# Optimization experiments

Hardware: AMD Instinct MI355X
Metric: run time of the kernel (lower is better)

The kernel has to match this reference:

```python
import jax, jax.numpy as jnp
import numpy as np

EPS = 1e-08  # matches torch default eps in both F.normalize and PairwiseDistance


def setup_inputs() -> dict:
    key = jax.random.key(0)
    x = jax.random.normal(key, (8192, 1024), dtype=jnp.float32)
    return {"x": x}


def reference(x) -> jnp.ndarray:
    B = x.shape[0]
    # F.normalize(x, p=2, dim=-1, eps=EPS): x / max(||x||_2, eps)
    norms = jnp.linalg.norm(x, axis=-1, keepdims=True)
    xn = x / jnp.maximum(norms, EPS)
    # cosine similarity matrix [B, B]
    cos_sim = xn @ xn.T
    # fill_diagonal_(-2): exclude self from nearest-neighbor search
    idx = jnp.arange(B)
    cos_sim = cos_sim.at[idx, idx].set(-2.0)
    nn_idx = jnp.argmax(cos_sim, axis=1)  # [B] int
    # torch PairwiseDistance(p=2, eps=EPS): ||x1 - x2 + eps||_2
    diff = xn - xn[nn_idx] + EPS
    nn_dist = jnp.sqrt(jnp.sum(diff * diff, axis=-1))  # [B]
    loss = -jnp.mean(jnp.log(nn_dist + EPS))
    return loss
```

## Files before the change

### kernel.cpp

```cpp
#include <hip/hip_runtime.h>
#include <hip/hip_bf16.h>
#include <math.h>

#define NB 8192
#define ND 1024
#define KEPS 1e-8f
#define SLOTS 128
#define NTILE 32
#define NWG 528
#define NKT 16

typedef __attribute__((ext_vector_type(8))) __bf16 bf16x8;
typedef __attribute__((ext_vector_type(4))) float f32x4;

__device__ __forceinline__ unsigned int fmono(float f) {
    unsigned int b = __float_as_uint(f);
    return b ^ ((b & 0x80000000u) ? 0xFFFFFFFFu : 0x80000000u);
}
__device__ __forceinline__ unsigned short f2bf(float f) {
    union { float f; unsigned int u; } a;
    a.f = f;
    unsigned int lsb = (a.u >> 16) & 1u;
    a.u += 0x7fffu + lsb;
    return (unsigned short)(a.u >> 16);
}
__device__ __forceinline__ void gload_lds16(const void* g, void* l) {
    __builtin_amdgcn_global_load_lds(
        (const __attribute__((address_space(1))) unsigned int*)g,
        (__attribute__((address_space(3))) unsigned int*)l, 16, 0, 0);
}
__device__ __forceinline__ unsigned long long packmax(float mx, int mc) {
    return ((unsigned long long)fmono(mx) << 32) |
           (unsigned long long)(~(unsigned int)mc);
}

__global__ __launch_bounds__(256) void normalize_k(const float* __restrict__ x,
                                                   unsigned short* __restrict__ xnb) {
    int row = blockIdx.x;
    int t = threadIdx.x;
    float4 v = ((const float4*)(x + (size_t)row * ND))[t];
    float ss = v.x * v.x + v.y * v.y + v.z * v.z + v.w * v.w;
#pragma unroll
    for (int off = 32; off > 0; off >>= 1) ss += __shfl_down(ss, off, 64);
    __shared__ float sred[4];
    if ((t & 63) == 0) sred[t >> 6] = ss;
    __syncthreads();
    float tot = sred[0] + sred[1] + sred[2] + sred[3];
    float scale = 1.0f / fmaxf(sqrtf(tot), KEPS);
    ushort4 o;
    o.x = f2bf(v.x * scale);
    o.y = f2bf(v.y * scale);
    o.z = f2bf(v.z * scale);
    o.w = f2bf(v.w * scale);
    ((ushort4*)xnb)[(size_t)row * (ND / 4) + t] = o;
}

#define FENCE_BARRIER() do { asm volatile("" ::: "memory"); \
    __builtin_amdgcn_s_barrier(); asm volatile("" ::: "memory"); } while (0)
#define WAIT_VM2() asm volatile("s_waitcnt vmcnt(2)" ::: "memory")
#define WAIT_VM0() asm volatile("s_waitcnt vmcnt(0)" ::: "memory")

#define STAGE_HALF(H, DBB) do { \
    gload_lds16(sp[H][0], ldsb + (DBB) + ((H) >> 1) * 32768 + ((H) & 1) * 16384 + (0 * 8 + wv) * 1024); \
    gload_lds16(sp[H][1], ldsb + (DBB) + ((H) >> 1) * 32768 + ((H) & 1) * 16384 + (1 * 8 + wv) * 1024); \
    sp[H][0] += 128; sp[H][1] += 128; } while (0)

#define LOAD_A(MH) do { \
    const char* Ab_ = ldsb + cbB + wM * 16384 + laneA; \
    _Pragma("unroll") for (int mi = 0; mi < 4; ++mi) \
    _Pragma("unroll") for (int ks = 0; ks < 2; ++ks) \
        af[mi][ks] = *(const bf16x8*)(Ab_ + ((((MH) * 4 + mi) * 2 + ks) * 1024)); } while (0)

#define LOAD_B(BANK, NH) do { \
    const char* Bb_ = ldsb + cbB + 32768 + (wN >> 1) * 16384 + laneA; \
    _Pragma("unroll") for (int ni = 0; ni < 2; ++ni) \
    _Pragma("unroll") for (int ks = 0; ks < 2; ++ks) \
        BANK[ni][ks] = *(const bf16x8*)(Bb_ + ((((wN & 1) * 4 + (NH) * 2 + ni) * 2 + ks) * 1024)); } while (0)

#define MFMAQ(MH, NH, BANK) do { \
    __builtin_amdgcn_s_setprio(1); \
    _Pragma("unroll") for (int mi = 0; mi < 4; ++mi) \
    _Pragma("unroll") for (int ni = 0; ni < 2; ++ni) { \
        acc[(MH) * 4 + mi][(NH) * 2 + ni] = __builtin_amdgcn_mfma_f32_16x16x32_bf16( \
            af[mi][0], BANK[ni][0], acc[(MH) * 4 + mi][(NH) * 2 + ni], 0, 0, 0); \
        acc[(MH) * 4 + mi][(NH) * 2 + ni] = __builtin_amdgcn_mfma_f32_16x16x32_bf16( \
            af[mi][1], BANK[ni][1], acc[(MH) * 4 + mi][(NH) * 2 + ni], 0, 0, 0); } \
    __builtin_amdgcn_s_setprio(0); } while (0)

__global__ __launch_bounds__(512, 2) void argmax_gemm(const unsigned short* __restrict__ xnb,
                                                      unsigned long long* __restrict__ partial) {
    extern __shared__ char ldsb[];

    int wg = (int)blockIdx.x;
    int tile = (wg & 7) * (NWG / 8) + (wg >> 3);
    int by = 0, tr = tile;
    while (tr >= NTILE - by) { tr -= NTILE - by; ++by; }
    const int bx = by + tr;

    const int rowBase = by * 256, colBase = bx * 256;
    const int tid = (int)threadIdx.x;
    const int wv = tid >> 6;
    const int l = tid & 63;
    const int wM = wv >> 2;
    const int wN = wv & 3;

    const int laneA = (l & 15) * 64 + (((l >> 4) * 16) ^ ((l & 8) << 2));

    const int scb = ((l & 3) * 16) ^ ((l >> 5) << 5);
    const int srow = (l >> 2) & 15;

    const char* xb = (const char*)xnb;
    const char* sp[4][2];
#pragma unroll
    for (int h = 0; h < 4; ++h)
#pragma unroll
        for (int q = 0; q < 2; ++q) {
            int s = q * 8 + wv;
            int rgrp = s >> 1, kgrp = s & 1;
            int panel = (h >> 1) ? colBase : rowBase;
            long long grow = panel + (h & 1) * 128 + rgrp * 16 + srow;
            sp[h][q] = xb + grow * (ND * 2) + kgrp * 64 + scb;
        }

    f32x4 acc[8][4];
#pragma unroll
    for (int m = 0; m < 8; ++m)
#pragma unroll
        for (int n = 0; n < 4; ++n) acc[m][n] = f32x4{0.f, 0.f, 0.f, 0.f};

    STAGE_HALF(0, 0); STAGE_HALF(1, 0); STAGE_HALF(2, 0); STAGE_HALF(3, 0);

    int cbB = 0, dbB = 65536;
    for (int c = 0; c < NKT; ++c) {
        const bool pf = (c + 1 < NKT);
        bf16x8 af[4][2], b0[2][2], b1[2][2];
        if (pf) { STAGE_HALF(0, dbB); WAIT_VM2(); } else { WAIT_VM0(); }
        FENCE_BARRIER();
        LOAD_A(0); LOAD_B(b0, 0);
        MFMAQ(0, 0, b0);
        if (pf) STAGE_HALF(1, dbB);
        LOAD_B(b1, 1);
        MFMAQ(0, 1, b1);
        if (pf) STAGE_HALF(2, dbB);
        LOAD_A(1);
        MFMAQ(1, 1, b1);
        if (pf) STAGE_HALF(3, dbB);
        MFMAQ(1, 0, b0);
        FENCE_BARRIER();
        int tmp = cbB; cbB = dbB; dbB = tmp;
    }

#pragma unroll
    for (int m = 0; m < 8; ++m) {
#pragma unroll
        for (int r = 0; r < 4; ++r) {
            int gi = rowBase + wM * 128 + m * 16 + (l >> 4) * 4 + r;
            float mx = -3.0f;
            int mc = 0x7FFFFFFF;
#pragma unroll
            for (int n = 0; n < 4; ++n) {
                int gj = colBase + wN * 64 + n * 16 + (l & 15);
                float v = (gi == gj) ? -2.0f : acc[m][n][r];
                if (v > mx) { mx = v; mc = gj; }
            }
#pragma unroll
            for (int off = 1; off < 16; off <<= 1) {
                float omx = __shfl_xor(mx, off, 64);
                int omc = __shfl_xor(mc, off, 64);
                if (omx > mx || (omx == mx && omc < mc)) { mx = omx; mc = omc; }
            }
            if ((l & 15) == 0)
                partial[(size_t)gi * SLOTS + (2 * by + (bx - by) * 4 + wN)] = packmax(mx, mc);
        }
    }
    if (bx > by) {
#pragma unroll
        for (int n = 0; n < 4; ++n) {
            int gj = colBase + wN * 64 + n * 16 + (l & 15);
            float mx = -3.0f;
            int mc = 0x7FFFFFFF;
#pragma unroll
            for (int m = 0; m < 8; ++m) {
#pragma unroll
                for (int r = 0; r < 4; ++r) {
                    int gi = rowBase + wM * 128 + m * 16 + (l >> 4) * 4 + r;
                    float v = (gi == gj) ? -2.0f : acc[m][n][r];
                    if (v > mx) { mx = v; mc = gi; }
                }
            }
#pragma unroll
            for (int off = 16; off < 64; off <<= 1) {
                float omx = __shfl_xor(mx, off, 64);
                int omc = __shfl_xor(mc, off, 64);
                if (omx > mx || (omx == mx && omc < mc)) { mx = omx; mc = omc; }
            }
            if ((l >> 4) == 0)
                partial[(size_t)gj * SLOTS + (2 * by + wM)] = packmax(mx, mc);
        }
    }
}

__global__ __launch_bounds__(256) void dist_k(const float* __restrict__ x,
                                              const unsigned long long* __restrict__ partial,
                                              float* __restrict__ rowloss) {
    int i = blockIdx.x;
    int t = threadIdx.x;
    int nv = SLOTS - 2 * (i >> 8);
    unsigned long long p = 0ull;
    if (t < nv) p = partial[(size_t)i * SLOTS + t];
#pragma unroll
    for (int off = 1; off < 64; off <<= 1) {
        unsigned long long o = __shfl_xor(p, off, 64);
        if (o > p) p = o;
    }
    __shared__ unsigned long long sp_[4];
    __shared__ int sj;
    if ((t & 63) == 0) sp_[t >> 6] = p;
    __syncthreads();
    if (t == 0) {
        unsigned long long b = sp_[0];
        for (int k = 1; k < 4; ++k)
            if (sp_[k] > b) b = sp_[k];
        sj = (int)(~(unsigned int)(b & 0xFFFFFFFFull));
    }
    __syncthreads();
    int j = sj;

    float4 a = ((const float4*)(x + (size_t)i * ND))[t];
    float4 b = ((const float4*)(x + (size_t)j * ND))[t];
    float sa = a.x * a.x + a.y * a.y + a.z * a.z + a.w * a.w;
    float sb = b.x * b.x + b.y * b.y + b.z * b.z + b.w * b.w;
#pragma unroll
    for (int off = 32; off > 0; off >>= 1) {
        sa += __shfl_down(sa, off, 64);
        sb += __shfl_down(sb, off, 64);
    }
    __shared__ float sra[4], srb[4];
    if ((t & 63) == 0) { sra[t >> 6] = sa; srb[t >> 6] = sb; }
    __syncthreads();
    float na = sra[0] + sra[1] + sra[2] + sra[3];
    float nb = srb[0] + srb[1] + srb[2] + srb[3];
    float ia = 1.0f / fmaxf(sqrtf(na), KEPS);
    float ib = 1.0f / fmaxf(sqrtf(nb), KEPS);
    float dx = a.x * ia - b.x * ib + KEPS;
    float dy = a.y * ia - b.y * ib + KEPS;
    float dz = a.z * ia - b.z * ib + KEPS;
    float dw = a.w * ia - b.w * ib + KEPS;
    float ss = dx * dx + dy * dy + dz * dz + dw * dw;
#pragma unroll
    for (int off = 32; off > 0; off >>= 1) ss += __shfl_down(ss, off, 64);
    __shared__ float srd[4];
    if ((t & 63) == 0) srd[t >> 6] = ss;
    __syncthreads();
    if (t == 0) {
        float tot = srd[0] + srd[1] + srd[2] + srd[3];
        rowloss[i] = -logf(sqrtf(tot) + KEPS);
    }
}

__global__ __launch_bounds__(1024) void reduce_k(const float* __restrict__ rowloss,
                                                 float* __restrict__ out) {
    int t = threadIdx.x;
    float s = 0.0f;
#pragma unroll
    for (int k = 0; k < 8; ++k) s += rowloss[t + k * 1024];
#pragma unroll
    for (int off = 32; off > 0; off >>= 1) s += __shfl_down(s, off, 64);
    __shared__ float sred[16];
    if ((t & 63) == 0) sred[t >> 6] = s;
    __syncthreads();
    if (t == 0) {
        float tot = 0.0f;
        for (int k = 0; k < 16; ++k) tot += sred[k];
        out[0] = tot / (float)NB;
    }
}

extern "C" void kernel_launch(void* const* d_in, const int* in_sizes, int n_in,
                              void* d_out, int out_size, void* d_ws, size_t ws_size,
                              hipStream_t stream) {
    const float* x = (const float*)d_in[0];
    float* out = (float*)d_out;

    char* ws = (char*)d_ws;
    unsigned short* xnb = (unsigned short*)ws;
    unsigned long long* partial =
        (unsigned long long*)(ws + (size_t)NB * ND * 2);
    float* rowloss = (float*)(ws + (size_t)NB * ND * 2 + (size_t)NB * SLOTS * 8);

    (void)hipFuncSetAttribute((const void*)argmax_gemm,
                              hipFuncAttributeMaxDynamicSharedMemorySize, 131072);

    normalize_k<<<NB, 256, 0, stream>>>(x, xnb);
    argmax_gemm<<<NWG, 512, 131072, stream>>>(xnb, partial);
    dist_k<<<NB, 256, 0, stream>>>(x, partial, rowloss);
    reduce_k<<<1, 1024, 0, stream>>>(rowloss, out);
}
```

Before: 209.6 us.

## Rework GEMM LDS layout and staging schedule; make normalize/dist one row per wave

The argmax GEMM gets a new LDS layout with an XOR swizzle and new per-lane row and k offsets. Its main loop is unrolled into explicit k-tile macros that interleave global-to-LDS staging with MFMA quarters, using extra barriers, explicit lgkmcnt waits and a deeper vmcnt wait to pipeline prefetch. The normalize and distance kernels now process one row per wavefront with four float4 loads per lane and shuffle-only reductions, removing shared-memory syncs and cutting block count. The many extra barriers and the hand-tuned wait counts risk stalls or hazards if the counts are wrong.

```diff
diff --git a/kernel.cpp b/kernel.cpp
--- a/kernel.cpp
+++ b/kernel.cpp
@@ -36,46 +36,54 @@
 
 __global__ __launch_bounds__(256) void normalize_k(const float* __restrict__ x,
                                                    unsigned short* __restrict__ xnb) {
-    int row = blockIdx.x;
-    int t = threadIdx.x;
-    float4 v = ((const float4*)(x + (size_t)row * ND))[t];
-    float ss = v.x * v.x + v.y * v.y + v.z * v.z + v.w * v.w;
-#pragma unroll
-    for (int off = 32; off > 0; off >>= 1) ss += __shfl_down(ss, off, 64);
-    __shared__ float sred[4];
-    if ((t & 63) == 0) sred[t >> 6] = ss;
-    __syncthreads();
-    float tot = sred[0] + sred[1] + sred[2] + sred[3];
-    float scale = 1.0f / fmaxf(sqrtf(tot), KEPS);
-    ushort4 o;
-    o.x = f2bf(v.x * scale);
-    o.y = f2bf(v.y * scale);
-    o.z = f2bf(v.z * scale);
-    o.w = f2bf(v.w * scale);
-    ((ushort4*)xnb)[(size_t)row * (ND / 4) + t] = o;
+    int row = blockIdx.x * 4 + (threadIdx.x >> 6);
+    int l = threadIdx.x & 63;
+    const float4* xr = (const float4*)(x + (size_t)row * ND);
+    float4 v[4];
+    float ss = 0.f;
+#pragma unroll
+    for (int q = 0; q < 4; ++q) {
+        v[q] = xr[q * 64 + l];
+        ss += v[q].x * v[q].x + v[q].y * v[q].y + v[q].z * v[q].z + v[q].w * v[q].w;
+    }
+#pragma unroll
+    for (int off = 1; off < 64; off <<= 1) ss += __shfl_xor(ss, off, 64);
+    float scale = 1.0f / fmaxf(sqrtf(ss), KEPS);
+    ushort4* o = (ushort4*)(xnb + (size_t)row * ND);
+#pragma unroll
+    for (int q = 0; q < 4; ++q) {
+        ushort4 u;
+        u.x = f2bf(v[q].x * scale);
+        u.y = f2bf(v[q].y * scale);
+        u.z = f2bf(v[q].z * scale);
+        u.w = f2bf(v[q].w * scale);
+        o[q * 64 + l] = u;
+    }
 }
 
 #define FENCE_BARRIER() do { asm volatile("" ::: "memory"); \
     __builtin_amdgcn_s_barrier(); asm volatile("" ::: "memory"); } while (0)
-#define WAIT_VM2() asm volatile("s_waitcnt vmcnt(2)" ::: "memory")
+#define LGKM0() do { asm volatile("s_waitcnt lgkmcnt(0)" ::: "memory"); \
+    __builtin_amdgcn_sched_barrier(0); } while (0)
+#define WAIT_VM6() asm volatile("s_waitcnt vmcnt(6)" ::: "memory")
 #define WAIT_VM0() asm volatile("s_waitcnt vmcnt(0)" ::: "memory")
 
-#define STAGE_HALF(H, DBB) do { \
-    gload_lds16(sp[H][0], ldsb + (DBB) + ((H) >> 1) * 32768 + ((H) & 1) * 16384 + (0 * 8 + wv) * 1024); \
-    gload_lds16(sp[H][1], ldsb + (DBB) + ((H) >> 1) * 32768 + ((H) & 1) * 16384 + (1 * 8 + wv) * 1024); \
+#define STAGE(H, DB) do { \
+    gload_lds16(sp[H][0], ldsb + (DB) + (H) * 16384 + wv * 1024); \
+    gload_lds16(sp[H][1], ldsb + (DB) + (H) * 16384 + 8192 + wv * 1024); \
     sp[H][0] += 128; sp[H][1] += 128; } while (0)
 
-#define LOAD_A(MH) do { \
-    const char* Ab_ = ldsb + cbB + wM * 16384 + laneA; \
-    _Pragma("unroll") for (int mi = 0; mi < 4; ++mi) \
-    _Pragma("unroll") for (int ks = 0; ks < 2; ++ks) \
-        af[mi][ks] = *(const bf16x8*)(Ab_ + ((((MH) * 4 + mi) * 2 + ks) * 1024)); } while (0)
-
-#define LOAD_B(BANK, NH) do { \
-    const char* Bb_ = ldsb + cbB + 32768 + (wN >> 1) * 16384 + laneA; \
-    _Pragma("unroll") for (int ni = 0; ni < 2; ++ni) \
-    _Pragma("unroll") for (int ks = 0; ks < 2; ++ks) \
-        BANK[ni][ks] = *(const bf16x8*)(Bb_ + ((((wN & 1) * 4 + (NH) * 2 + ni) * 2 + ks) * 1024)); } while (0)
+#define LOAD_A(CB, MQ) do { \
+    const char* Ab_ = ldsb + (CB) + ((MQ) * 2 + wM) * 8192 + rowOff; \
+    _Pragma("unroll") for (int mi = 0; mi < 4; ++mi) { \
+        af[mi][0] = *(const bf16x8*)(Ab_ + mi * 2048 + ks0); \
+        af[mi][1] = *(const bf16x8*)(Ab_ + mi * 2048 + ks1); } } while (0)
+
+#define LOAD_B(CB, BANK, NQ) do { \
+    const char* Bb_ = ldsb + (CB) + 32768 + (NQ) * 16384 + wN * 4096 + rowOff; \
+    _Pragma("unroll") for (int ni = 0; ni < 2; ++ni) { \
+        BANK[ni][0] = *(const bf16x8*)(Bb_ + ni * 2048 + ks0); \
+        BANK[ni][1] = *(const bf16x8*)(Bb_ + ni * 2048 + ks1); } } while (0)
 
 #define MFMAQ(MH, NH, BANK) do { \
     __builtin_amdgcn_s_setprio(1); \
@@ -87,6 +95,32 @@
             af[mi][1], BANK[ni][1], acc[(MH) * 4 + mi][(NH) * 2 + ni], 0, 0, 0); } \
     __builtin_amdgcn_s_setprio(0); } while (0)
 
+#define KTILE(CB, DB, S1, S2, FINAL) do { \
+    bf16x8 af[4][2], b0[2][2], b1[2][2]; \
+    LOAD_A(CB, 0); LOAD_B(CB, b0, 0); \
+    if (S1) STAGE(1, DB); \
+    FENCE_BARRIER(); LGKM0(); MFMAQ(0, 0, b0); FENCE_BARRIER(); \
+    LOAD_B(CB, b1, 1); \
+    if (S2) STAGE(0, CB); \
+    FENCE_BARRIER(); LGKM0(); MFMAQ(0, 1, b1); FENCE_BARRIER(); \
+    LOAD_A(CB, 1); \
+    if (S2) STAGE(2, CB); \
+    FENCE_BARRIER(); LGKM0(); MFMAQ(1, 1, b1); FENCE_BARRIER(); \
+    if (S2) STAGE(3, CB); \
+    FENCE_BARRIER(); MFMAQ(1, 0, b0); \
+    if (FINAL) { WAIT_VM0(); } else { WAIT_VM6(); } \
+    FENCE_BARRIER(); } while (0)
+
+#define KTILE_LAST(CB) do { \
+    bf16x8 af[4][2], b0[2][2], b1[2][2]; \
+    LOAD_A(CB, 0); LOAD_B(CB, b0, 0); \
+    FENCE_BARRIER(); LGKM0(); MFMAQ(0, 0, b0); FENCE_BARRIER(); \
+    LOAD_B(CB, b1, 1); \
+    FENCE_BARRIER(); LGKM0(); MFMAQ(0, 1, b1); FENCE_BARRIER(); \
+    LOAD_A(CB, 1); \
+    FENCE_BARRIER(); LGKM0(); MFMAQ(1, 1, b1); FENCE_BARRIER(); \
+    MFMAQ(1, 0, b0); } while (0)
+
 __global__ __launch_bounds__(512, 2) void argmax_gemm(const unsigned short* __restrict__ xnb,
                                                       unsigned long long* __restrict__ partial) {
     extern __shared__ char ldsb[];
@@ -104,23 +138,23 @@
     const int wM = wv >> 2;
     const int wN = wv & 3;
 
-    const int laneA = (l & 15) * 64 + (((l >> 4) * 16) ^ ((l & 8) << 2));
-
-    const int scb = ((l & 3) * 16) ^ ((l >> 5) << 5);
-    const int srow = (l >> 2) & 15;
-
+    const int rowOff = (l & 15) * 128;
+    const int ks0 = (((l >> 4) * 16)) ^ ((l & 7) << 4);
+    const int ks1 = (64 | ((l >> 4) * 16)) ^ ((l & 7) << 4);
+
+    const int scol = (((l & 7) ^ (l >> 3)) << 4);
     const char* xb = (const char*)xnb;
     const char* sp[4][2];
 #pragma unroll
-    for (int h = 0; h < 4; ++h)
-#pragma unroll
-        for (int q = 0; q < 2; ++q) {
-            int s = q * 8 + wv;
-            int rgrp = s >> 1, kgrp = s & 1;
-            int panel = (h >> 1) ? colBase : rowBase;
-            long long grow = panel + (h & 1) * 128 + rgrp * 16 + srow;
-            sp[h][q] = xb + grow * (ND * 2) + kgrp * 64 + scb;
-        }
+    for (int q = 0; q < 2; ++q) {
+        int R = (q * 8 + wv) * 8 + (l >> 3);
+        int arow = (R >> 6) * 128 + (R & 63);
+        int bcol = (R >> 5) * 64 + (R & 31);
+        sp[0][q] = xb + (size_t)(rowBase + arow) * 2048 + scol;
+        sp[1][q] = xb + (size_t)(rowBase + arow + 64) * 2048 + scol;
+        sp[2][q] = xb + (size_t)(colBase + bcol) * 2048 + scol;
+        sp[3][q] = xb + (size_t)(colBase + bcol + 32) * 2048 + scol;
+    }
 
     f32x4 acc[8][4];
 #pragma unroll
@@ -128,27 +162,19 @@
 #pragma unroll
         for (int n = 0; n < 4; ++n) acc[m][n] = f32x4{0.f, 0.f, 0.f, 0.f};
 
-    STAGE_HALF(0, 0); STAGE_HALF(1, 0); STAGE_HALF(2, 0); STAGE_HALF(3, 0);
-
-    int cbB = 0, dbB = 65536;
-    for (int c = 0; c < NKT; ++c) {
-        const bool pf = (c + 1 < NKT);
-        bf16x8 af[4][2], b0[2][2], b1[2][2];
-        if (pf) { STAGE_HALF(0, dbB); WAIT_VM2(); } else { WAIT_VM0(); }
-        FENCE_BARRIER();
-        LOAD_A(0); LOAD_B(b0, 0);
-        MFMAQ(0, 0, b0);
-        if (pf) STAGE_HALF(1, dbB);
-        LOAD_B(b1, 1);
-        MFMAQ(0, 1, b1);
-        if (pf) STAGE_HALF(2, dbB);
-        LOAD_A(1);
-        MFMAQ(1, 1, b1);
-        if (pf) STAGE_HALF(3, dbB);
-        MFMAQ(1, 0, b0);
-        FENCE_BARRIER();
-        int tmp = cbB; cbB = dbB; dbB = tmp;
-    }
+    STAGE(0, 0); STAGE(2, 0); STAGE(3, 0); STAGE(1, 0);
+    STAGE(0, 65536); STAGE(2, 65536); STAGE(3, 65536);
+    WAIT_VM6();
+    FENCE_BARRIER();
+
+    for (int c = 0; c < 12; c += 2) {
+        KTILE(0, 65536, true, true, false);
+        KTILE(65536, 0, true, true, false);
+    }
+    KTILE(0, 65536, true, true, false);
+    KTILE(65536, 0, true, true, false);
+    KTILE(0, 65536, true, false, true);
+    KTILE_LAST(65536);
 
 #pragma unroll
     for (int m = 0; m < 8; ++m) {
@@ -203,59 +229,52 @@
 __global__ __launch_bounds__(256) void dist_k(const float* __restrict__ x,
                                               const unsigned long long* __restrict__ partial,
                                               float* __restrict__ rowloss) {
-    int i = blockIdx.x;
-    int t = threadIdx.x;
+    int i = blockIdx.x * 4 + (threadIdx.x >> 6);
+    int l = threadIdx.x & 63;
     int nv = SLOTS - 2 * (i >> 8);
     unsigned long long p = 0ull;
-    if (t < nv) p = partial[(size_t)i * SLOTS + t];
+    if (l < nv) p = partial[(size_t)i * SLOTS + l];
+    if (l + 64 < nv) {
+        unsigned long long o = partial[(size_t)i * SLOTS + l + 64];
+        if (o > p) p = o;
+    }
 #pragma unroll
     for (int off = 1; off < 64; off <<= 1) {
         unsigned long long o = __shfl_xor(p, off, 64);
         if (o > p) p = o;
     }
-    __shared__ unsigned long long sp_[4];
-    __shared__ int sj;
-    if ((t & 63) == 0) sp_[t >> 6] = p;
-    __syncthreads();
-    if (t == 0) {
-        unsigned long long b = sp_[0];
-        for (int k = 1; k < 4; ++k)
-            if (sp_[k] > b) b = sp_[k];
-        sj = (int)(~(unsigned int)(b & 0xFFFFFFFFull));
-    }
-    __syncthreads();
-    int j = sj;
-
-    float4 a = ((const float4*)(x + (size_t)i * ND))[t];
-    float4 b = ((const float4*)(x + (size_t)j * ND))[t];
-    float sa = a.x * a.x + a.y * a.y + a.z * a.z + a.w * a.w;
-    float sb = b.x * b.x + b.y * b.y + b.z * b.z + b.w * b.w;
-#pragma unroll
-    for (int off = 32; off > 0; off >>= 1) {
-        sa += __shfl_down(sa, off, 64);
-        sb += __shfl_down(sb, off, 64);
-    }
-    __shared__ float sra[4], srb[4];
-    if ((t & 63) == 0) { sra[t >> 6] = sa; srb[t >> 6] = sb; }
-    __syncthreads();
-    float na = sra[0] + sra[1] + sra[2] + sra[3];
-    float nb = srb[0] + srb[1] + srb[2] + srb[3];
-    float ia = 1.0f / fmaxf(sqrtf(na), KEPS);
-    float ib = 1.0f / fmaxf(sqrtf(nb), KEPS);
-    float dx = a.x * ia - b.x * ib + KEPS;
-    float dy = a.y * ia - b.y * ib + KEPS;
-    float dz = a.z * ia - b.z * ib + KEPS;
-    float dw = a.w * ia - b.w * ib + KEPS;
-    float ss = dx * dx + dy * dy + dz * dz + dw * dw;
-#pragma unroll
-    for (int off = 32; off > 0; off >>= 1) ss += __shfl_down(ss, off, 64);
-    __shared__ float srd[4];
-    if ((t & 63) == 0) srd[t >> 6] = ss;
-    __syncthreads();
-    if (t == 0) {
-        float tot = srd[0] + srd[1] + srd[2] + srd[3];
-        rowloss[i] = -logf(sqrtf(tot) + KEPS);
-    }
+    int j = (int)(~(unsigned int)(p & 0xFFFFFFFFull));
+
+    const float4* xi = (const float4*)(x + (size_t)i * ND);
+    const float4* xj = (const float4*)(x + (size_t)j * ND);
+    float4 a[4], b[4];
+    float sa = 0.f, sb = 0.f;
+#pragma unroll
+    for (int q = 0; q < 4; ++q) {
+        a[q] = xi[q * 64 + l];
+        b[q] = xj[q * 64 + l];
+        sa += a[q].x * a[q].x + a[q].y * a[q].y + a[q].z * a[q].z + a[q].w * a[q].w;
+        sb += b[q].x * b[q].x + b[q].y * b[q].y + b[q].z * b[q].z + b[q].w * b[q].w;
+    }
+#pragma unroll
+    for (int off = 1; off < 64; off <<= 1) {
+        sa += __shfl_xor(sa, off, 64);
+        sb += __shfl_xor(sb, off, 64);
+    }
+    float ia = 1.0f / fmaxf(sqrtf(sa), KEPS);
+    float ib = 1.0f / fmaxf(sqrtf(sb), KEPS);
+    float ss = 0.f;
+#pragma unroll
+    for (int q = 0; q < 4; ++q) {
+        float dx = a[q].x * ia - b[q].x * ib + KEPS;
+        float dy = a[q].y * ia - b[q].y * ib + KEPS;
+        float dz = a[q].z * ia - b[q].z * ib + KEPS;
+        float dw = a[q].w * ia - b[q].w * ib + KEPS;
+        ss += dx * dx + dy * dy + dz * dz + dw * dw;
+    }
+#pragma unroll
+    for (int off = 1; off < 64; off <<= 1) ss += __shfl_xor(ss, off, 64);
+    if (l == 0) rowloss[i] = -logf(sqrtf(ss) + KEPS);
 }
 
 __global__ __launch_bounds__(1024) void reduce_k(const float* __restrict__ rowloss,
@@ -291,8 +310,8 @@
     (void)hipFuncSetAttribute((const void*)argmax_gemm,
                               hipFuncAttributeMaxDynamicSharedMemorySize, 131072);
 
-    normalize_k<<<NB, 256, 0, stream>>>(x, xnb);
+    normalize_k<<<NB / 4, 256, 0, stream>>>(x, xnb);
     argmax_gemm<<<NWG, 512, 131072, stream>>>(xnb, partial);
-    dist_k<<<NB, 256, 0, stream>>>(x, partial, rowloss);
+    dist_k<<<NB / 4, 256, 0, stream>>>(x, partial, rowloss);
     reduce_k<<<1, 1024, 0, stream>>>(rowloss, out);
 }
```

Result: slower. 217.6 us (+3.8%).
